# Optimization experiments

Measured on AMD Instinct MI355X. Metric: run time of the kernel, lower is better.

## Reference

```python
import jax, jax.numpy as jnp
import numpy as np

B, S, D = 1, 2048, 4096
H, KV = 32, 8
HD = D // H  # 128
NEG = -1e9


def _rope(t, cos, sin):
    # t: [B,S,h,HD]; cos/sin: [S,HD//2] -> broadcast [1,S,1,HD//2]
    tr = t[..., 0::2]
    ti = t[..., 1::2]
    c = cos[None, :, None, :]
    s = sin[None, :, None, :]
    out_r = tr * c - ti * s
    out_i = tr * s + ti * c
    # interleave back: (..., HD//2, 2) -> (..., HD)
    return jnp.stack([out_r, out_i], axis=-1).reshape(t.shape)


def setup_inputs() -> dict:
    key = jax.random.key(0)
    ks = jax.random.split(key, 5)
    w_scale = 0.02
    x = jax.random.normal(ks[0], (B, S, D), dtype=jnp.float32)
    wq = jax.random.normal(ks[1], (H * HD, D), dtype=jnp.float32) * w_scale
    wk = jax.random.normal(ks[2], (KV * HD, D), dtype=jnp.float32) * w_scale
    wv = jax.random.normal(ks[3], (KV * HD, D), dtype=jnp.float32) * w_scale
    wo = jax.random.normal(ks[4], (D, H * HD), dtype=jnp.float32) * w_scale
    # RoPE tables (theta = 10000)
    inv_freq = 1.0 / (10000.0 ** (np.arange(0, HD, 2, dtype=np.float32) / HD))
    angles = np.arange(S, dtype=np.float32)[:, None] * inv_freq[None, :]  # [S, HD//2]
    freqs_cos = jnp.asarray(np.cos(angles))
    freqs_sin = jnp.asarray(np.sin(angles))
    # causal additive mask [1,1,S,S]
    causal = jnp.tril(jnp.ones((S, S), dtype=bool))
    mask = jnp.where(causal, 0.0, NEG).astype(jnp.float32)[None, None]
    return {"x": x, "wq": wq, "wk": wk, "wv": wv, "wo": wo,
            "freqs_cos": freqs_cos, "freqs_sin": freqs_sin, "mask": mask}


def reference(x, wq, wk, wv, wo, freqs_cos, freqs_sin, mask):
    b, s, d = x.shape
    q = (x @ wq.T).reshape(b, s, H, HD)
    k = (x @ wk.T).reshape(b, s, KV, HD)
    v = (x @ wv.T).reshape(b, s, KV, HD)
    q = _rope(q, freqs_cos, freqs_sin)
    k = _rope(k, freqs_cos, freqs_sin)
    rep = H // KV
    k = jnp.repeat(k, rep, axis=2)  # [b,s,H,HD]
    v = jnp.repeat(v, rep, axis=2)
    scores = jnp.einsum('bshd,bthd->bhst', q, k) / jnp.sqrt(jnp.float32(HD))
    scores = scores + mask
    attn = jax.nn.softmax(scores, axis=-1)
    out = jnp.einsum('bhst,bthd->bshd', attn, v).reshape(b, s, H * HD)
    return out @ wo.T
```

## Files before the change

### kernel.cpp

```cpp
#include <hip/hip_runtime.h>
#include <hip/hip_bf16.h>
#include <math.h>

#define SEQ 2048
#define DIM 4096
#define NH 32
#define NKV 8
#define HD 128
#define KVD 1024
#define SCALE 0.08838834764831845f
#define NEGBIG -1000000000.0f

typedef __bf16 bf16;
typedef __attribute__((ext_vector_type(4))) __bf16 bf16x4;
typedef __attribute__((ext_vector_type(8))) __bf16 bf16x8;
typedef __attribute__((ext_vector_type(4))) float f32x4;

__device__ __forceinline__ void async_g2l16(const bf16* g, bf16* l) {
  __builtin_amdgcn_global_load_lds(
      (const __attribute__((address_space(1))) void*)g,
      (__attribute__((address_space(3))) void*)l,
      16, 0, 0);
}

#define SEG_X  2097152
#define SEG_WQ 4194304
#define SEG_WK 1048576
#define C0 SEG_X
#define C1 (C0 + SEG_WQ)
#define C2 (C1 + SEG_WK)
#define C3 (C2 + SEG_WK)
#define C4 (C3 + SEG_WQ)

__global__ void cast_all_kernel(const float* __restrict__ x,
                                const float* __restrict__ wq,
                                const float* __restrict__ wk,
                                const float* __restrict__ wv,
                                const float* __restrict__ wo,
                                bf16* __restrict__ xb, bf16* __restrict__ wqb,
                                bf16* __restrict__ wkb, bf16* __restrict__ wvb,
                                bf16* __restrict__ wob) {
  int i = blockIdx.x * 256 + threadIdx.x;
  const float* src; bf16* dst; int j;
  if (i < C0)      { src = x;  dst = xb;  j = i; }
  else if (i < C1) { src = wq; dst = wqb; j = i - C0; }
  else if (i < C2) { src = wk; dst = wkb; j = i - C1; }
  else if (i < C3) { src = wv; dst = wvb; j = i - C2; }
  else             { src = wo; dst = wob; j = i - C3; }
  float4 v = ((const float4*)src)[j];
  bf16x4 o;
  o[0] = (bf16)v.x; o[1] = (bf16)v.y; o[2] = (bf16)v.z; o[3] = (bf16)v.w;
  ((bf16x4*)dst)[j] = o;
}

#define BAR()       asm volatile("s_barrier" ::: "memory")
#define FENCE4()    asm volatile("s_waitcnt vmcnt(4)" ::: "memory")
#define FENCE_ALL() asm volatile("s_waitcnt vmcnt(0)" ::: "memory")

#define MFMAQ(AH, BC, MO, NO)                                              \
  _Pragma("unroll") for (int m2 = 0; m2 < 4; ++m2)                         \
  _Pragma("unroll") for (int n2 = 0; n2 < 2; ++n2)                         \
  _Pragma("unroll") for (int kk = 0; kk < 2; ++kk)                         \
    acc[(MO) + m2][(NO) + n2] = __builtin_amdgcn_mfma_f32_16x16x32_bf16(   \
        (AH)[m2][kk], (BC)[n2][kk], acc[(MO) + m2][(NO) + n2], 0, 0, 0);

__device__ __forceinline__ void gemm256_core(
    const bf16* __restrict__ Ag,
    const bf16* __restrict__ Bg,
    f32x4 acc[8][4])
{
  __shared__ __align__(16) bf16 As[2 * 256 * 64];
  __shared__ __align__(16) bf16 Bs[2 * 256 * 64];

  const int tid  = threadIdx.x;
  const int lane = tid & 63;
  const int w    = tid >> 6;
  const int l15  = lane & 15;
  const int quad = lane >> 4;
  const int wr2  = (w >> 2) * 128;
  const int wc2  = (w & 3) * 64;

  const int srow = w * 8 + (lane >> 3);
  const int sg8  = ((lane & 7) ^ (lane >> 3)) * 8;
  const bf16* gA = Ag + (size_t)srow * DIM + sg8;
  const bf16* gB = Bg + (size_t)srow * DIM + sg8;
  bf16* lA = As + w * 512;
  bf16* lB = Bs + w * 512;

  const int g0   = (quad ^ (l15 & 7)) * 8;
  const int g1   = g0 ^ 32;
  const int aOff = (wr2 + l15) * 64;
  const int bOff = (wc2 + l15) * 64;

#define STAGE_A(b, kt)                                                     \
  { _Pragma("unroll") for (int hh = 0; hh < 2; ++hh)                       \
    _Pragma("unroll") for (int j = 0; j < 2; ++j)                          \
      async_g2l16(gA + (size_t)(hh * 128 + j * 64) * DIM + (kt) * 64,      \
                  lA + (b) * 16384 + (hh * 128 + j * 64) * 64); }
#define STAGE_B0(b, kt)                                                    \
  { _Pragma("unroll") for (int j = 0; j < 2; ++j)                          \
      async_g2l16(gB + (size_t)(j * 64) * DIM + (kt) * 64,                 \
                  lB + (b) * 16384 + (j * 64) * 64); }
#define STAGE_B1(b, kt)                                                    \
  { _Pragma("unroll") for (int j = 0; j < 2; ++j)                          \
      async_g2l16(gB + (size_t)(128 + j * 64) * DIM + (kt) * 64,           \
                  lB + (b) * 16384 + (128 + j * 64) * 64); }

#define LDA(b, rh, m2, gk) \
  (*(const bf16x8*)(As + (b) * 16384 + aOff + (rh) * 4096 + (m2) * 1024 + (gk)))
#define LDB(b, ch, n2, gk) \
  (*(const bf16x8*)(Bs + (b) * 16384 + bOff + (ch) * 2048 + (n2) * 1024 + (gk)))

  const f32x4 vz = {0.f, 0.f, 0.f, 0.f};
#pragma unroll
  for (int mi = 0; mi < 8; ++mi)
#pragma unroll
    for (int ni = 0; ni < 4; ++ni) acc[mi][ni] = vz;

  STAGE_A(0, 0); STAGE_B0(0, 0); STAGE_B1(0, 0);
  STAGE_B0(1, 1); STAGE_B1(1, 1);
  FENCE4();
  BAR();

  for (int i = 0; i < 32; ++i) {
    const int ktn0 = (2 * i + 2 > 63) ? 63 : 2 * i + 2;
    const int ktn1 = (2 * i + 3 > 63) ? 63 : 2 * i + 3;
    {
      bf16x8 aH[4][2], bC0[2][2], bC1[2][2];
#pragma unroll
      for (int m2 = 0; m2 < 4; ++m2) { aH[m2][0] = LDA(0, 0, m2, g0); aH[m2][1] = LDA(0, 0, m2, g1); }
#pragma unroll
      for (int n2 = 0; n2 < 2; ++n2) { bC0[n2][0] = LDB(0, 0, n2, g0); bC0[n2][1] = LDB(0, 0, n2, g1); }
      STAGE_A(1, 2 * i + 1);
      BAR(); __builtin_amdgcn_s_setprio(1);
      MFMAQ(aH, bC0, 0, 0);
      __builtin_amdgcn_s_setprio(0); BAR();
#pragma unroll
      for (int n2 = 0; n2 < 2; ++n2) { bC1[n2][0] = LDB(0, 1, n2, g0); bC1[n2][1] = LDB(0, 1, n2, g1); }
      BAR(); __builtin_amdgcn_s_setprio(1);
      MFMAQ(aH, bC1, 0, 2);
      __builtin_amdgcn_s_setprio(0); BAR();
#pragma unroll
      for (int m2 = 0; m2 < 4; ++m2) { aH[m2][0] = LDA(0, 1, m2, g0); aH[m2][1] = LDA(0, 1, m2, g1); }
      STAGE_B0(0, ktn0);
      BAR(); __builtin_amdgcn_s_setprio(1);
      MFMAQ(aH, bC1, 4, 2);
      __builtin_amdgcn_s_setprio(0); BAR();
      STAGE_B1(0, ktn0);
      FENCE4();
      BAR(); __builtin_amdgcn_s_setprio(1);
      MFMAQ(aH, bC0, 4, 0);
      __builtin_amdgcn_s_setprio(0); BAR();
    }
    {
      bf16x8 aH[4][2], bC0[2][2], bC1[2][2];
#pragma unroll
      for (int m2 = 0; m2 < 4; ++m2) { aH[m2][0] = LDA(1, 0, m2, g0); aH[m2][1] = LDA(1, 0, m2, g1); }
#pragma unroll
      for (int n2 = 0; n2 < 2; ++n2) { bC0[n2][0] = LDB(1, 0, n2, g0); bC0[n2][1] = LDB(1, 0, n2, g1); }
      STAGE_A(0, ktn0);
      BAR(); __builtin_amdgcn_s_setprio(1);
      MFMAQ(aH, bC0, 0, 0);
      __builtin_amdgcn_s_setprio(0); BAR();
#pragma unroll
      for (int n2 = 0; n2 < 2; ++n2) { bC1[n2][0] = LDB(1, 1, n2, g0); bC1[n2][1] = LDB(1, 1, n2, g1); }
      BAR(); __builtin_amdgcn_s_setprio(1);
      MFMAQ(aH, bC1, 0, 2);
      __builtin_amdgcn_s_setprio(0); BAR();
#pragma unroll
      for (int m2 = 0; m2 < 4; ++m2) { aH[m2][0] = LDA(1, 1, m2, g0); aH[m2][1] = LDA(1, 1, m2, g1); }
      STAGE_B0(1, ktn1);
      BAR(); __builtin_amdgcn_s_setprio(1);
      MFMAQ(aH, bC1, 4, 2);
      __builtin_amdgcn_s_setprio(0); BAR();
      STAGE_B1(1, ktn1);
      FENCE4();
      BAR(); __builtin_amdgcn_s_setprio(1);
      MFMAQ(aH, bC0, 4, 0);
      __builtin_amdgcn_s_setprio(0); BAR();
    }
  }
  FENCE_ALL();
}

__global__ __launch_bounds__(512, 2) void qkv256_kernel(
    const bf16* __restrict__ xb, const bf16* __restrict__ wqb,
    const bf16* __restrict__ wkb, const bf16* __restrict__ wvb,
    const float* __restrict__ fc, const float* __restrict__ fs,
    bf16* __restrict__ Qb, bf16* __restrict__ Kb, bf16* __restrict__ Vt)
{
  const int bid   = blockIdx.x;
  const int mTile = bid & 7;
  const int nTile = bid >> 3;
  const bf16* Bg;
  if (nTile < 16)      Bg = wqb + (size_t)nTile * 256 * DIM;
  else if (nTile < 20) Bg = wkb + (size_t)(nTile - 16) * 256 * DIM;
  else                 Bg = wvb + (size_t)(nTile - 20) * 256 * DIM;

  f32x4 acc[8][4];
  gemm256_core(xb + (size_t)mTile * 256 * DIM, Bg, acc);

  const int tid  = threadIdx.x;
  const int lane = tid & 63;
  const int w    = tid >> 6;
  const int l15  = lane & 15;
  const int quad = lane >> 4;
  const int wr2  = (w >> 2) * 128;
  const int wc2  = (w & 3) * 64;
  const int sBase = mTile * 256 + wr2 + quad * 4;
  const int nBase = nTile * 256 + wc2;

  if (nTile < 20) {
    const bool isQ = nTile < 16;
    bf16* dst      = isQ ? Qb : Kb;
    const int ldd  = isQ ? DIM : KVD;
    const float sc = isQ ? SCALE : 1.0f;
    const int cOff = isQ ? nBase : nBase - 4096;
    const int odd  = l15 & 1;
#pragma unroll
    for (int mi = 0; mi < 8; ++mi)
#pragma unroll
      for (int ni = 0; ni < 4; ++ni) {
        const int n    = nBase + ni * 16 + l15;
        const int fidx = (n >> 1) & 63;
        const int col  = cOff + ni * 16 + l15;
#pragma unroll
        for (int r = 0; r < 4; ++r) {
          const int s = sBase + mi * 16 + r;
          float v  = acc[mi][ni][r];
          float pv = __shfl_xor(v, 1, 64);
          float c  = fc[s * 64 + fidx];
          float sn = fs[s * 64 + fidx];
          float o  = odd ? (pv * sn + v * c) : (v * c - pv * sn);
          dst[(size_t)s * ldd + col] = (bf16)(o * sc);
        }
      }
  } else {
    const int vBase = nBase - 5120;
#pragma unroll
    for (int mi = 0; mi < 8; ++mi) {
      const int sb = sBase + mi * 16;
#pragma unroll
      for (int ni = 0; ni < 4; ++ni) {
        const int nv = vBase + ni * 16 + l15;
        const int t = nv >> 7, d = nv & 127;
        bf16x4 pv;
#pragma unroll
        for (int r = 0; r < 4; ++r) pv[r] = (bf16)acc[mi][ni][r];
        *(bf16x4*)(Vt + ((size_t)t * HD + d) * SEQ + sb) = pv;
      }
    }
  }
}

__global__ __launch_bounds__(512, 2) void out256_kernel(
    const bf16* __restrict__ attnb, const bf16* __restrict__ wob,
    float* __restrict__ out)
{
  const int bid   = blockIdx.x;
  const int mTile = bid & 7;
  const int nTile = bid >> 3;

  f32x4 acc[8][4];
  gemm256_core(attnb + (size_t)mTile * 256 * DIM,
               wob + (size_t)nTile * 256 * DIM, acc);

  const int tid  = threadIdx.x;
  const int lane = tid & 63;
  const int w    = tid >> 6;
  const int l15  = lane & 15;
  const int quad = lane >> 4;
  const int wr2  = (w >> 2) * 128;
  const int wc2  = (w & 3) * 64;
  const int sBase = mTile * 256 + wr2 + quad * 4;
#pragma unroll
  for (int mi = 0; mi < 8; ++mi)
#pragma unroll
    for (int ni = 0; ni < 4; ++ni) {
      const int col = nTile * 256 + wc2 + ni * 16 + l15;
#pragma unroll
      for (int r = 0; r < 4; ++r)
        out[(size_t)(sBase + mi * 16 + r) * DIM + col] = acc[mi][ni][r];
    }
}

__global__ __launch_bounds__(256, 2) void attn_kernel(
    const bf16* __restrict__ Qb, const bf16* __restrict__ Kb,
    const bf16* __restrict__ Vt, bf16* __restrict__ attnb)
{
  __shared__ __align__(16) bf16 Ks[64 * 128];
  __shared__ __align__(16) bf16 Vs[128 * 64];
  __shared__ __align__(16) bf16 Ps[128 * 64];

  const int b    = blockIdx.x;
  const int half = b >> 8;
  const int r8   = b & 255;
  const int h    = (half << 4) | (r8 >> 4);
  const int qt   = half ? (r8 & 15) : 15 - (r8 & 15);
  const int kvh  = h >> 2;
  const int qbase = qt * 128;

  const int tid  = threadIdx.x;
  const int lane = tid & 63;
  const int w    = tid >> 6;
  const int l15  = lane & 15;
  const int quad = lane >> 4;

  bf16x8 qfrag[2][4];
#pragma unroll
  for (int n = 0; n < 2; ++n) {
    int q = qbase + w * 32 + n * 16 + l15;
#pragma unroll
    for (int ks = 0; ks < 4; ++ks)
      qfrag[n][ks] = *(const bf16x8*)(Qb + (size_t)q * DIM + h * HD +
                                      ks * 32 + quad * 8);
  }

  const f32x4 vzero = {0.f, 0.f, 0.f, 0.f};
  f32x4 oacc[8][2];
#pragma unroll
  for (int dm = 0; dm < 8; ++dm)
#pragma unroll
    for (int n = 0; n < 2; ++n) oacc[dm][n] = vzero;
  float m_run[2] = {-1e30f, -1e30f};
  float l_run[2] = {0.f, 0.f};

  const int nkt = 2 * (qt + 1);
  for (int kt = 0; kt < nkt; ++kt) {
    const int kbase = kt * 64;

    __syncthreads();
#pragma unroll
    for (int t = 0; t < 4; ++t) {
      int kr0 = w * 16 + t * 4;
      int krow = kr0 + (lane >> 4);
      int kg = (lane & 15) ^ (krow & 7);
      async_g2l16(Kb + (size_t)(kbase + krow) * KVD + kvh * HD + kg * 8,
                  Ks + kr0 * 128);
      int vr0 = w * 32 + t * 8;
      int d = vr0 + (lane >> 3);
      int vg = (lane & 7) ^ (d & 7);
      async_g2l16(Vt + ((size_t)kvh * HD + d) * SEQ + kbase + vg * 8,
                  Vs + vr0 * 64);
    }
    __syncthreads();

    f32x4 sacc[4][2];
#pragma unroll
    for (int kg = 0; kg < 4; ++kg)
#pragma unroll
      for (int n = 0; n < 2; ++n) sacc[kg][n] = vzero;
#pragma unroll
    for (int kg = 0; kg < 4; ++kg) {
      bf16x8 kf[4];
#pragma unroll
      for (int ks = 0; ks < 4; ++ks) {
        int row = kg * 16 + l15;
        kf[ks] = *(const bf16x8*)(Ks + row * 128 +
                                  (((ks * 4 + quad) ^ (row & 7)) * 8));
      }
#pragma unroll
      for (int n = 0; n < 2; ++n)
#pragma unroll
        for (int ks = 0; ks < 4; ++ks)
          sacc[kg][n] = __builtin_amdgcn_mfma_f32_16x16x32_bf16(
              kf[ks], qfrag[n][ks], sacc[kg][n], 0, 0, 0);
    }

#pragma unroll
    for (int n = 0; n < 2; ++n) {
      const int qloc = w * 32 + n * 16 + l15;
      const int qglob = qbase + qloc;
      if (kbase + 63 > qbase + w * 32 + n * 16) {
#pragma unroll
        for (int kg = 0; kg < 4; ++kg)
#pragma unroll
          for (int r = 0; r < 4; ++r) {
            int key = kbase + kg * 16 + quad * 4 + r;
            if (key > qglob) sacc[kg][n][r] = NEGBIG;
          }
      }
      float mx = -1e30f;
#pragma unroll
      for (int kg = 0; kg < 4; ++kg)
#pragma unroll
        for (int r = 0; r < 4; ++r) mx = fmaxf(mx, sacc[kg][n][r]);
      mx = fmaxf(mx, __shfl_xor(mx, 16, 64));
      mx = fmaxf(mx, __shfl_xor(mx, 32, 64));
      float mnew = fmaxf(m_run[n], mx);
      float alpha = __expf(m_run[n] - mnew);
      m_run[n] = mnew;
      float rs = 0.f;
#pragma unroll
      for (int kg = 0; kg < 4; ++kg) {
        bf16x4 pk;
#pragma unroll
        for (int r = 0; r < 4; ++r) {
          float p = __expf(sacc[kg][n][r] - mnew);
          rs += p;
          pk[r] = (bf16)p;
        }
        int g16 = (kg * 2 + (quad >> 1)) ^ (qloc & 7);
        *(bf16x4*)(Ps + qloc * 64 + g16 * 8 + (quad & 1) * 4) = pk;
      }
      rs += __shfl_xor(rs, 16, 64);
      rs += __shfl_xor(rs, 32, 64);
      l_run[n] = alpha * l_run[n] + rs;
#pragma unroll
      for (int dm = 0; dm < 8; ++dm)
#pragma unroll
        for (int r = 0; r < 4; ++r) oacc[dm][n][r] *= alpha;
    }

    bf16x8 pf[2][2];
#pragma unroll
    for (int kk = 0; kk < 2; ++kk)
#pragma unroll
      for (int n = 0; n < 2; ++n) {
        int qloc = w * 32 + n * 16 + l15;
        pf[kk][n] = *(const bf16x8*)(Ps + qloc * 64 +
                                     (((kk * 4 + quad) ^ (qloc & 7)) * 8));
      }
#pragma unroll
    for (int dm = 0; dm < 8; ++dm) {
#pragma unroll
      for (int kk = 0; kk < 2; ++kk) {
        int d = dm * 16 + l15;
        bf16x8 vf = *(const bf16x8*)(Vs + d * 64 +
                                     (((kk * 4 + quad) ^ (d & 7)) * 8));
#pragma unroll
        for (int n = 0; n < 2; ++n)
          oacc[dm][n] = __builtin_amdgcn_mfma_f32_16x16x32_bf16(
              vf, pf[kk][n], oacc[dm][n], 0, 0, 0);
      }
    }
  }

#pragma unroll
  for (int n = 0; n < 2; ++n) {
    float inv = 1.0f / l_run[n];
    int q = qbase + w * 32 + n * 16 + l15;
#pragma unroll
    for (int dm = 0; dm < 8; ++dm) {
      bf16x4 ov;
#pragma unroll
      for (int r = 0; r < 4; ++r) ov[r] = (bf16)(oacc[dm][n][r] * inv);
      *(bf16x4*)(attnb + (size_t)q * DIM + h * HD + dm * 16 + quad * 4) = ov;
    }
  }
}

extern "C" void kernel_launch(void* const* d_in, const int* in_sizes, int n_in,
                              void* d_out, int out_size, void* d_ws, size_t ws_size,
                              hipStream_t stream) {
  const float* x  = (const float*)d_in[0];
  const float* wq = (const float*)d_in[1];
  const float* wk = (const float*)d_in[2];
  const float* wv = (const float*)d_in[3];
  const float* wo = (const float*)d_in[4];
  const float* fc = (const float*)d_in[5];
  const float* fs = (const float*)d_in[6];
  float* out = (float*)d_out;

  size_t off = 0;
  char* wsb = (char*)d_ws;
  auto take = [&](size_t bytes) -> void* {
    void* p = wsb + off;
    off += (bytes + 255) & ~(size_t)255;
    return p;
  };
  bf16*  xb    = (bf16*)take((size_t)SEQ * DIM * 2);
  bf16*  wqb   = (bf16*)take((size_t)DIM * DIM * 2);
  bf16*  wkb   = (bf16*)take((size_t)KVD * DIM * 2);
  bf16*  wvb   = (bf16*)take((size_t)KVD * DIM * 2);
  bf16*  wob   = (bf16*)take((size_t)DIM * DIM * 2);
  bf16*  Qb    = (bf16*)take((size_t)SEQ * DIM * 2);
  bf16*  Kb    = (bf16*)take((size_t)SEQ * KVD * 2);
  bf16*  Vt    = (bf16*)take((size_t)NKV * HD * SEQ * 2);
  bf16*  attnb = (bf16*)take((size_t)SEQ * DIM * 2);

  cast_all_kernel<<<C4 / 256, 256, 0, stream>>>(x, wq, wk, wv, wo,
                                                xb, wqb, wkb, wvb, wob);

  qkv256_kernel<<<dim3(192), 512, 0, stream>>>(xb, wqb, wkb, wvb,
                                               fc, fs, Qb, Kb, Vt);

  attn_kernel<<<dim3(512), 256, 0, stream>>>(Qb, Kb, Vt, attnb);

  out256_kernel<<<dim3(128), 512, 0, stream>>>(attnb, wob, out);
}
```

Measured before the change: 511.7 us.

## Narrow GEMM N-tiles so QKV and output projections launch 256 blocks

```diff
diff --git a/kernel.cpp b/kernel.cpp
--- a/kernel.cpp
+++ b/kernel.cpp
@@ -26,11 +26,11 @@
 #define SEG_X  2097152
 #define SEG_WQ 4194304
 #define SEG_WK 1048576
-#define C0 SEG_X
-#define C1 (C0 + SEG_WQ)
-#define C2 (C1 + SEG_WK)
-#define C3 (C2 + SEG_WK)
-#define C4 (C3 + SEG_WQ)
+#define C0SEG SEG_X
+#define C1SEG (C0SEG + SEG_WQ)
+#define C2SEG (C1SEG + SEG_WK)
+#define C3SEG (C2SEG + SEG_WK)
+#define C4SEG (C3SEG + SEG_WQ)
 
 __global__ void cast_all_kernel(const float* __restrict__ x,
                                 const float* __restrict__ wq,
@@ -42,11 +42,11 @@
                                 bf16* __restrict__ wob) {
   int i = blockIdx.x * 256 + threadIdx.x;
   const float* src; bf16* dst; int j;
-  if (i < C0)      { src = x;  dst = xb;  j = i; }
-  else if (i < C1) { src = wq; dst = wqb; j = i - C0; }
-  else if (i < C2) { src = wk; dst = wkb; j = i - C1; }
-  else if (i < C3) { src = wv; dst = wvb; j = i - C2; }
-  else             { src = wo; dst = wob; j = i - C3; }
+  if (i < C0SEG)      { src = x;  dst = xb;  j = i; }
+  else if (i < C1SEG) { src = wq; dst = wqb; j = i - C0SEG; }
+  else if (i < C2SEG) { src = wk; dst = wkb; j = i - C1SEG; }
+  else if (i < C3SEG) { src = wv; dst = wvb; j = i - C2SEG; }
+  else                { src = wo; dst = wob; j = i - C3SEG; }
   float4 v = ((const float4*)src)[j];
   bf16x4 o;
   o[0] = (bf16)v.x; o[1] = (bf16)v.y; o[2] = (bf16)v.z; o[3] = (bf16)v.w;
@@ -54,23 +54,18 @@
 }
 
 #define BAR()       asm volatile("s_barrier" ::: "memory")
-#define FENCE4()    asm volatile("s_waitcnt vmcnt(4)" ::: "memory")
 #define FENCE_ALL() asm volatile("s_waitcnt vmcnt(0)" ::: "memory")
 
-#define MFMAQ(AH, BC, MO, NO)                                              \
-  _Pragma("unroll") for (int m2 = 0; m2 < 4; ++m2)                         \
-  _Pragma("unroll") for (int n2 = 0; n2 < 2; ++n2)                         \
-  _Pragma("unroll") for (int kk = 0; kk < 2; ++kk)                         \
-    acc[(MO) + m2][(NO) + n2] = __builtin_amdgcn_mfma_f32_16x16x32_bf16(   \
-        (AH)[m2][kk], (BC)[n2][kk], acc[(MO) + m2][(NO) + n2], 0, 0, 0);
-
+template<int NF>
 __device__ __forceinline__ void gemm256_core(
     const bf16* __restrict__ Ag,
     const bf16* __restrict__ Bg,
-    f32x4 acc[8][4])
+    f32x4 acc[8][NF])
 {
+  constexpr int C0F  = NF - (NF >> 1);
+  constexpr int BUFB = NF * 4096;
   __shared__ __align__(16) bf16 As[2 * 256 * 64];
-  __shared__ __align__(16) bf16 Bs[2 * 256 * 64];
+  __shared__ __align__(16) bf16 Bs[2 * BUFB];
 
   const int tid  = threadIdx.x;
   const int lane = tid & 63;
@@ -78,7 +73,7 @@
   const int l15  = lane & 15;
   const int quad = lane >> 4;
   const int wr2  = (w >> 2) * 128;
-  const int wc2  = (w & 3) * 64;
+  const int wc3  = (w & 3) * (16 * NF);
 
   const int srow = w * 8 + (lane >> 3);
   const int sg8  = ((lane & 7) ^ (lane >> 3)) * 8;
@@ -90,115 +85,119 @@
   const int g0   = (quad ^ (l15 & 7)) * 8;
   const int g1   = g0 ^ 32;
   const int aOff = (wr2 + l15) * 64;
-  const int bOff = (wc2 + l15) * 64;
-
-#define STAGE_A(b, kt)                                                     \
-  { _Pragma("unroll") for (int hh = 0; hh < 2; ++hh)                       \
-    _Pragma("unroll") for (int j = 0; j < 2; ++j)                          \
-      async_g2l16(gA + (size_t)(hh * 128 + j * 64) * DIM + (kt) * 64,      \
-                  lA + (b) * 16384 + (hh * 128 + j * 64) * 64); }
-#define STAGE_B0(b, kt)                                                    \
-  { _Pragma("unroll") for (int j = 0; j < 2; ++j)                          \
-      async_g2l16(gB + (size_t)(j * 64) * DIM + (kt) * 64,                 \
-                  lB + (b) * 16384 + (j * 64) * 64); }
-#define STAGE_B1(b, kt)                                                    \
-  { _Pragma("unroll") for (int j = 0; j < 2; ++j)                          \
-      async_g2l16(gB + (size_t)(128 + j * 64) * DIM + (kt) * 64,           \
-                  lB + (b) * 16384 + (128 + j * 64) * 64); }
-
-#define LDA(b, rh, m2, gk) \
-  (*(const bf16x8*)(As + (b) * 16384 + aOff + (rh) * 4096 + (m2) * 1024 + (gk)))
-#define LDB(b, ch, n2, gk) \
-  (*(const bf16x8*)(Bs + (b) * 16384 + bOff + (ch) * 2048 + (n2) * 1024 + (gk)))
+  const int bOff = (wc3 + l15) * 64;
+
+  auto stageA = [&](int b, int kt) {
+#pragma unroll
+    for (int j = 0; j < 4; ++j)
+      async_g2l16(gA + (size_t)(j * 64) * DIM + kt * 64,
+                  lA + b * 16384 + j * 4096);
+  };
+  auto stageB = [&](int b, int kt) {
+#pragma unroll
+    for (int j = 0; j < NF; ++j)
+      async_g2l16(gB + (size_t)(j * 64) * DIM + kt * 64,
+                  lB + b * BUFB + j * 4096);
+  };
+  auto fence_steady = [] {
+    if constexpr (NF == 3) asm volatile("s_waitcnt vmcnt(7)" ::: "memory");
+    else                   asm volatile("s_waitcnt vmcnt(6)" ::: "memory");
+  };
 
   const f32x4 vz = {0.f, 0.f, 0.f, 0.f};
 #pragma unroll
   for (int mi = 0; mi < 8; ++mi)
 #pragma unroll
-    for (int ni = 0; ni < 4; ++ni) acc[mi][ni] = vz;
-
-  STAGE_A(0, 0); STAGE_B0(0, 0); STAGE_B1(0, 0);
-  STAGE_B0(1, 1); STAGE_B1(1, 1);
-  FENCE4();
+    for (int ni = 0; ni < NF; ++ni) acc[mi][ni] = vz;
+
+  auto ktile = [&](int b, int kt2) {
+    const bf16* Ab = As + b * 16384;
+    const bf16* Bb = Bs + b * BUFB;
+    bf16x8 aH[4][2], bc0[C0F][2], bc1[2];
+#pragma unroll
+    for (int m2 = 0; m2 < 4; ++m2) {
+      aH[m2][0] = *(const bf16x8*)(Ab + aOff + m2 * 1024 + g0);
+      aH[m2][1] = *(const bf16x8*)(Ab + aOff + m2 * 1024 + g1);
+    }
+#pragma unroll
+    for (int n = 0; n < C0F; ++n) {
+      bc0[n][0] = *(const bf16x8*)(Bb + bOff + n * 1024 + g0);
+      bc0[n][1] = *(const bf16x8*)(Bb + bOff + n * 1024 + g1);
+    }
+    BAR(); __builtin_amdgcn_s_setprio(1);
+#pragma unroll
+    for (int m2 = 0; m2 < 4; ++m2)
+#pragma unroll
+      for (int n = 0; n < C0F; ++n)
+#pragma unroll
+        for (int kk = 0; kk < 2; ++kk)
+          acc[m2][n] = __builtin_amdgcn_mfma_f32_16x16x32_bf16(
+              aH[m2][kk], bc0[n][kk], acc[m2][n], 0, 0, 0);
+    __builtin_amdgcn_s_setprio(0); BAR();
+    bc1[0] = *(const bf16x8*)(Bb + bOff + C0F * 1024 + g0);
+    bc1[1] = *(const bf16x8*)(Bb + bOff + C0F * 1024 + g1);
+    BAR(); __builtin_amdgcn_s_setprio(1);
+#pragma unroll
+    for (int m2 = 0; m2 < 4; ++m2)
+#pragma unroll
+      for (int kk = 0; kk < 2; ++kk)
+        acc[m2][C0F] = __builtin_amdgcn_mfma_f32_16x16x32_bf16(
+            aH[m2][kk], bc1[kk], acc[m2][C0F], 0, 0, 0);
+    __builtin_amdgcn_s_setprio(0); BAR();
+#pragma unroll
+    for (int m2 = 0; m2 < 4; ++m2) {
+      aH[m2][0] = *(const bf16x8*)(Ab + aOff + 4096 + m2 * 1024 + g0);
+      aH[m2][1] = *(const bf16x8*)(Ab + aOff + 4096 + m2 * 1024 + g1);
+    }
+    stageB(b, kt2);
+    BAR(); __builtin_amdgcn_s_setprio(1);
+#pragma unroll
+    for (int m2 = 0; m2 < 4; ++m2)
+#pragma unroll
+      for (int kk = 0; kk < 2; ++kk)
+        acc[4 + m2][C0F] = __builtin_amdgcn_mfma_f32_16x16x32_bf16(
+            aH[m2][kk], bc1[kk], acc[4 + m2][C0F], 0, 0, 0);
+    __builtin_amdgcn_s_setprio(0); BAR();
+    stageA(b, kt2);
+    fence_steady();
+    BAR(); __builtin_amdgcn_s_setprio(1);
+#pragma unroll
+    for (int m2 = 0; m2 < 4; ++m2)
+#pragma unroll
+      for (int n = 0; n < C0F; ++n)
+#pragma unroll
+        for (int kk = 0; kk < 2; ++kk)
+          acc[4 + m2][n] = __builtin_amdgcn_mfma_f32_16x16x32_bf16(
+              aH[m2][kk], bc0[n][kk], acc[4 + m2][n], 0, 0, 0);
+    __builtin_amdgcn_s_setprio(0); BAR();
+  };
+
+  stageB(0, 0); stageA(0, 0); stageB(1, 1); stageA(1, 1);
+  fence_steady();
   BAR();
 
-  for (int i = 0; i < 32; ++i) {
-    const int ktn0 = (2 * i + 2 > 63) ? 63 : 2 * i + 2;
-    const int ktn1 = (2 * i + 3 > 63) ? 63 : 2 * i + 3;
-    {
-      bf16x8 aH[4][2], bC0[2][2], bC1[2][2];
-#pragma unroll
-      for (int m2 = 0; m2 < 4; ++m2) { aH[m2][0] = LDA(0, 0, m2, g0); aH[m2][1] = LDA(0, 0, m2, g1); }
-#pragma unroll
-      for (int n2 = 0; n2 < 2; ++n2) { bC0[n2][0] = LDB(0, 0, n2, g0); bC0[n2][1] = LDB(0, 0, n2, g1); }
-      STAGE_A(1, 2 * i + 1);
-      BAR(); __builtin_amdgcn_s_setprio(1);
-      MFMAQ(aH, bC0, 0, 0);
-      __builtin_amdgcn_s_setprio(0); BAR();
-#pragma unroll
-      for (int n2 = 0; n2 < 2; ++n2) { bC1[n2][0] = LDB(0, 1, n2, g0); bC1[n2][1] = LDB(0, 1, n2, g1); }
-      BAR(); __builtin_amdgcn_s_setprio(1);
-      MFMAQ(aH, bC1, 0, 2);
-      __builtin_amdgcn_s_setprio(0); BAR();
-#pragma unroll
-      for (int m2 = 0; m2 < 4; ++m2) { aH[m2][0] = LDA(0, 1, m2, g0); aH[m2][1] = LDA(0, 1, m2, g1); }
-      STAGE_B0(0, ktn0);
-      BAR(); __builtin_amdgcn_s_setprio(1);
-      MFMAQ(aH, bC1, 4, 2);
-      __builtin_amdgcn_s_setprio(0); BAR();
-      STAGE_B1(0, ktn0);
-      FENCE4();
-      BAR(); __builtin_amdgcn_s_setprio(1);
-      MFMAQ(aH, bC0, 4, 0);
-      __builtin_amdgcn_s_setprio(0); BAR();
-    }
-    {
-      bf16x8 aH[4][2], bC0[2][2], bC1[2][2];
-#pragma unroll
-      for (int m2 = 0; m2 < 4; ++m2) { aH[m2][0] = LDA(1, 0, m2, g0); aH[m2][1] = LDA(1, 0, m2, g1); }
-#pragma unroll
-      for (int n2 = 0; n2 < 2; ++n2) { bC0[n2][0] = LDB(1, 0, n2, g0); bC0[n2][1] = LDB(1, 0, n2, g1); }
-      STAGE_A(0, ktn0);
-      BAR(); __builtin_amdgcn_s_setprio(1);
-      MFMAQ(aH, bC0, 0, 0);
-      __builtin_amdgcn_s_setprio(0); BAR();
-#pragma unroll
-      for (int n2 = 0; n2 < 2; ++n2) { bC1[n2][0] = LDB(1, 1, n2, g0); bC1[n2][1] = LDB(1, 1, n2, g1); }
-      BAR(); __builtin_amdgcn_s_setprio(1);
-      MFMAQ(aH, bC1, 0, 2);
-      __builtin_amdgcn_s_setprio(0); BAR();
-#pragma unroll
-      for (int m2 = 0; m2 < 4; ++m2) { aH[m2][0] = LDA(1, 1, m2, g0); aH[m2][1] = LDA(1, 1, m2, g1); }
-      STAGE_B0(1, ktn1);
-      BAR(); __builtin_amdgcn_s_setprio(1);
-      MFMAQ(aH, bC1, 4, 2);
-      __builtin_amdgcn_s_setprio(0); BAR();
-      STAGE_B1(1, ktn1);
-      FENCE4();
-      BAR(); __builtin_amdgcn_s_setprio(1);
-      MFMAQ(aH, bC0, 4, 0);
-      __builtin_amdgcn_s_setprio(0); BAR();
-    }
+#pragma unroll 1
+  for (int t = 0; t < 64; t += 2) {
+    const int k2a = (t + 2 < 64) ? t + 2 : 63;
+    const int k2b = (t + 3 < 64) ? t + 3 : 63;
+    ktile(0, k2a);
+    ktile(1, k2b);
   }
   FENCE_ALL();
 }
 
 __global__ __launch_bounds__(512, 2) void qkv256_kernel(
-    const bf16* __restrict__ xb, const bf16* __restrict__ wqb,
-    const bf16* __restrict__ wkb, const bf16* __restrict__ wvb,
+    const bf16* __restrict__ xb, const bf16* __restrict__ wqkv,
     const float* __restrict__ fc, const float* __restrict__ fs,
     bf16* __restrict__ Qb, bf16* __restrict__ Kb, bf16* __restrict__ Vt)
 {
   const int bid   = blockIdx.x;
   const int mTile = bid & 7;
   const int nTile = bid >> 3;
-  const bf16* Bg;
-  if (nTile < 16)      Bg = wqb + (size_t)nTile * 256 * DIM;
-  else if (nTile < 20) Bg = wkb + (size_t)(nTile - 16) * 256 * DIM;
-  else                 Bg = wvb + (size_t)(nTile - 20) * 256 * DIM;
-
-  f32x4 acc[8][4];
-  gemm256_core(xb + (size_t)mTile * 256 * DIM, Bg, acc);
+
+  f32x4 acc[8][3];
+  gemm256_core<3>(xb + (size_t)mTile * 256 * DIM,
+                  wqkv + (size_t)nTile * 192 * DIM, acc);
 
   const int tid  = threadIdx.x;
   const int lane = tid & 63;
@@ -206,24 +205,24 @@
   const int l15  = lane & 15;
   const int quad = lane >> 4;
   const int wr2  = (w >> 2) * 128;
-  const int wc2  = (w & 3) * 64;
+  const int wc3  = (w & 3) * 48;
   const int sBase = mTile * 256 + wr2 + quad * 4;
-  const int nBase = nTile * 256 + wc2;
-
-  if (nTile < 20) {
-    const bool isQ = nTile < 16;
-    bf16* dst      = isQ ? Qb : Kb;
-    const int ldd  = isQ ? DIM : KVD;
-    const float sc = isQ ? SCALE : 1.0f;
-    const int cOff = isQ ? nBase : nBase - 4096;
-    const int odd  = l15 & 1;
-#pragma unroll
-    for (int mi = 0; mi < 8; ++mi)
-#pragma unroll
-      for (int ni = 0; ni < 4; ++ni) {
-        const int n    = nBase + ni * 16 + l15;
-        const int fidx = (n >> 1) & 63;
-        const int col  = cOff + ni * 16 + l15;
+  const int nBase = nTile * 192 + wc3;
+  const int odd  = l15 & 1;
+
+#pragma unroll
+  for (int ni = 0; ni < 3; ++ni) {
+    const int c16 = nBase + ni * 16;
+    const int col = c16 + l15;
+    if (c16 < 5120) {
+      const bool isQ = c16 < 4096;
+      bf16* dst      = isQ ? Qb : Kb;
+      const int ldd  = isQ ? DIM : KVD;
+      const float sc = isQ ? SCALE : 1.0f;
+      const int cc   = isQ ? col : col - 4096;
+      const int fidx = (col >> 1) & 63;
+#pragma unroll
+      for (int mi = 0; mi < 8; ++mi) {
 #pragma unroll
         for (int r = 0; r < 4; ++r) {
           const int s = sBase + mi * 16 + r;
@@ -232,22 +231,18 @@
           float c  = fc[s * 64 + fidx];
           float sn = fs[s * 64 + fidx];
           float o  = odd ? (pv * sn + v * c) : (v * c - pv * sn);
-          dst[(size_t)s * ldd + col] = (bf16)(o * sc);
+          dst[(size_t)s * ldd + cc] = (bf16)(o * sc);
         }
       }
-  } else {
-    const int vBase = nBase - 5120;
-#pragma unroll
-    for (int mi = 0; mi < 8; ++mi) {
-      const int sb = sBase + mi * 16;
-#pragma unroll
-      for (int ni = 0; ni < 4; ++ni) {
-        const int nv = vBase + ni * 16 + l15;
-        const int t = nv >> 7, d = nv & 127;
+    } else {
+      const int cv = col - 5120;
+      const int t = cv >> 7, d = cv & 127;
+#pragma unroll
+      for (int mi = 0; mi < 8; ++mi) {
         bf16x4 pv;
 #pragma unroll
         for (int r = 0; r < 4; ++r) pv[r] = (bf16)acc[mi][ni][r];
-        *(bf16x4*)(Vt + ((size_t)t * HD + d) * SEQ + sb) = pv;
+        *(bf16x4*)(Vt + ((size_t)t * HD + d) * SEQ + sBase + mi * 16) = pv;
       }
     }
   }
@@ -261,9 +256,9 @@
   const int mTile = bid & 7;
   const int nTile = bid >> 3;
 
-  f32x4 acc[8][4];
-  gemm256_core(attnb + (size_t)mTile * 256 * DIM,
-               wob + (size_t)nTile * 256 * DIM, acc);
+  f32x4 acc[8][2];
+  gemm256_core<2>(attnb + (size_t)mTile * 256 * DIM,
+                  wob + (size_t)nTile * 128 * DIM, acc);
 
   const int tid  = threadIdx.x;
   const int lane = tid & 63;
@@ -271,13 +266,14 @@
   const int l15  = lane & 15;
   const int quad = lane >> 4;
   const int wr2  = (w >> 2) * 128;
-  const int wc2  = (w & 3) * 64;
+  const int wc3  = (w & 3) * 32;
   const int sBase = mTile * 256 + wr2 + quad * 4;
+  const int cBase = nTile * 128 + wc3;
 #pragma unroll
   for (int mi = 0; mi < 8; ++mi)
 #pragma unroll
-    for (int ni = 0; ni < 4; ++ni) {
-      const int col = nTile * 256 + wc2 + ni * 16 + l15;
+    for (int ni = 0; ni < 2; ++ni) {
+      const int col = cBase + ni * 16 + l15;
 #pragma unroll
       for (int r = 0; r < 4; ++r)
         out[(size_t)(sBase + mi * 16 + r) * DIM + col] = acc[mi][ni][r];
@@ -479,13 +475,12 @@
   bf16*  Vt    = (bf16*)take((size_t)NKV * HD * SEQ * 2);
   bf16*  attnb = (bf16*)take((size_t)SEQ * DIM * 2);
 
-  cast_all_kernel<<<C4 / 256, 256, 0, stream>>>(x, wq, wk, wv, wo,
-                                                xb, wqb, wkb, wvb, wob);
-
-  qkv256_kernel<<<dim3(192), 512, 0, stream>>>(xb, wqb, wkb, wvb,
-                                               fc, fs, Qb, Kb, Vt);
+  cast_all_kernel<<<C4SEG / 256, 256, 0, stream>>>(x, wq, wk, wv, wo,
+                                                   xb, wqb, wkb, wvb, wob);
+
+  qkv256_kernel<<<dim3(256), 512, 0, stream>>>(xb, wqb, fc, fs, Qb, Kb, Vt);
 
   attn_kernel<<<dim3(512), 256, 0, stream>>>(Qb, Kb, Vt, attnb);
 
-  out256_kernel<<<dim3(128), 512, 0, stream>>>(attnb, wob, out);
-}
+  out256_kernel<<<dim3(256), 512, 0, stream>>>(attnb, wob, out);
+}
```

Result: faster. 491.6 us (-3.9%).

## Overlap wo cast with QKV GEMM and retile output GEMM to 128x128

Applied to the files above, without the earlier changes.

```diff
diff --git a/kernel.cpp b/kernel.cpp
--- a/kernel.cpp
+++ b/kernel.cpp
@@ -26,27 +26,23 @@
 #define SEG_X  2097152
 #define SEG_WQ 4194304
 #define SEG_WK 1048576
-#define C0 SEG_X
-#define C1 (C0 + SEG_WQ)
-#define C2 (C1 + SEG_WK)
-#define C3 (C2 + SEG_WK)
-#define C4 (C3 + SEG_WQ)
+#define CX0 SEG_X
+#define CX1 (CX0 + SEG_WQ)
+#define CX2 (CX1 + SEG_WK)
+#define CX3 (CX2 + SEG_WK)
 
 __global__ void cast_all_kernel(const float* __restrict__ x,
                                 const float* __restrict__ wq,
                                 const float* __restrict__ wk,
                                 const float* __restrict__ wv,
-                                const float* __restrict__ wo,
                                 bf16* __restrict__ xb, bf16* __restrict__ wqb,
-                                bf16* __restrict__ wkb, bf16* __restrict__ wvb,
-                                bf16* __restrict__ wob) {
+                                bf16* __restrict__ wkb, bf16* __restrict__ wvb) {
   int i = blockIdx.x * 256 + threadIdx.x;
   const float* src; bf16* dst; int j;
-  if (i < C0)      { src = x;  dst = xb;  j = i; }
-  else if (i < C1) { src = wq; dst = wqb; j = i - C0; }
-  else if (i < C2) { src = wk; dst = wkb; j = i - C1; }
-  else if (i < C3) { src = wv; dst = wvb; j = i - C2; }
-  else             { src = wo; dst = wob; j = i - C3; }
+  if (i < CX0)      { src = x;  dst = xb;  j = i; }
+  else if (i < CX1) { src = wq; dst = wqb; j = i - CX0; }
+  else if (i < CX2) { src = wk; dst = wkb; j = i - CX1; }
+  else              { src = wv; dst = wvb; j = i - CX2; }
   float4 v = ((const float4*)src)[j];
   bf16x4 o;
   o[0] = (bf16)v.x; o[1] = (bf16)v.y; o[2] = (bf16)v.z; o[3] = (bf16)v.w;
@@ -186,10 +182,21 @@
 __global__ __launch_bounds__(512, 2) void qkv256_kernel(
     const bf16* __restrict__ xb, const bf16* __restrict__ wqb,
     const bf16* __restrict__ wkb, const bf16* __restrict__ wvb,
+    const float* __restrict__ wo, bf16* __restrict__ wob,
     const float* __restrict__ fc, const float* __restrict__ fs,
     bf16* __restrict__ Qb, bf16* __restrict__ Kb, bf16* __restrict__ Vt)
 {
-  const int bid   = blockIdx.x;
+  const int bid = blockIdx.x;
+  const int tid = threadIdx.x;
+  if (bid >= 192) {
+    for (int j = (bid - 192) * 512 + tid; j < SEG_WQ; j += 64 * 512) {
+      float4 v = ((const float4*)wo)[j];
+      bf16x4 o;
+      o[0] = (bf16)v.x; o[1] = (bf16)v.y; o[2] = (bf16)v.z; o[3] = (bf16)v.w;
+      ((bf16x4*)wob)[j] = o;
+    }
+    return;
+  }
   const int mTile = bid & 7;
   const int nTile = bid >> 3;
   const bf16* Bg;
@@ -200,7 +207,6 @@
   f32x4 acc[8][4];
   gemm256_core(xb + (size_t)mTile * 256 * DIM, Bg, acc);
 
-  const int tid  = threadIdx.x;
   const int lane = tid & 63;
   const int w    = tid >> 6;
   const int l15  = lane & 15;
@@ -253,35 +259,94 @@
   }
 }
 
-__global__ __launch_bounds__(512, 2) void out256_kernel(
-    const bf16* __restrict__ attnb, const bf16* __restrict__ wob,
-    float* __restrict__ out)
+__device__ __forceinline__ void gemm128_core(
+    const bf16* __restrict__ A, int lda,
+    const bf16* __restrict__ B, int ldb,
+    int K, int mBase, f32x4 acc[4][4])
 {
-  const int bid   = blockIdx.x;
-  const int mTile = bid & 7;
-  const int nTile = bid >> 3;
-
-  f32x4 acc[8][4];
-  gemm256_core(attnb + (size_t)mTile * 256 * DIM,
-               wob + (size_t)nTile * 256 * DIM, acc);
+  __shared__ __align__(16) bf16 As[128 * 32];
+  __shared__ __align__(16) bf16 Bs[128 * 32];
 
   const int tid  = threadIdx.x;
   const int lane = tid & 63;
   const int w    = tid >> 6;
   const int l15  = lane & 15;
   const int quad = lane >> 4;
-  const int wr2  = (w >> 2) * 128;
-  const int wc2  = (w & 3) * 64;
-  const int sBase = mTile * 256 + wr2 + quad * 4;
-#pragma unroll
-  for (int mi = 0; mi < 8; ++mi)
+  const int wr   = (w >> 1) * 64;
+  const int wc   = (w & 1) * 64;
+
+  const int srow = lane >> 2;
+  const int kswz = ((lane & 3) ^ ((srow >> 1) & 3)) * 8;
+  const bf16* gA0 = A + (size_t)(mBase + w * 16 + srow) * lda + kswz;
+  const bf16* gA1 = gA0 + (size_t)64 * lda;
+  const bf16* gB0 = B + (size_t)(w * 16 + srow) * ldb + kswz;
+  const bf16* gB1 = gB0 + (size_t)64 * ldb;
+  bf16* lA0 = As + w * 512;
+  bf16* lA1 = As + (w + 4) * 512;
+  bf16* lB0 = Bs + w * 512;
+  bf16* lB1 = Bs + (w + 4) * 512;
+
+  const f32x4 vzero = {0.f, 0.f, 0.f, 0.f};
+#pragma unroll
+  for (int mi = 0; mi < 4; ++mi)
+#pragma unroll
+    for (int ni = 0; ni < 4; ++ni) acc[mi][ni] = vzero;
+
+  const int rsw = ((l15 >> 1) & 3);
+
+  for (int k0 = 0; k0 < K; k0 += 32) {
+    __syncthreads();
+    async_g2l16(gA0 + k0, lA0);
+    async_g2l16(gA1 + k0, lA1);
+    async_g2l16(gB0 + k0, lB0);
+    async_g2l16(gB1 + k0, lB1);
+    __syncthreads();
+
+    bf16x8 a[4], b[4];
+#pragma unroll
+    for (int mi = 0; mi < 4; ++mi)
+      a[mi] = *(const bf16x8*)(As + (wr + mi * 16 + l15) * 32 +
+                               ((quad ^ rsw) * 8));
+#pragma unroll
+    for (int ni = 0; ni < 4; ++ni)
+      b[ni] = *(const bf16x8*)(Bs + (wc + ni * 16 + l15) * 32 +
+                               ((quad ^ rsw) * 8));
+#pragma unroll
+    for (int mi = 0; mi < 4; ++mi)
+#pragma unroll
+      for (int ni = 0; ni < 4; ++ni)
+        acc[mi][ni] = __builtin_amdgcn_mfma_f32_16x16x32_bf16(
+            a[mi], b[ni], acc[mi][ni], 0, 0, 0);
+  }
+}
+
+__global__ __launch_bounds__(256, 2) void out_gemm_kernel(
+    const bf16* __restrict__ attnb, const bf16* __restrict__ wob,
+    float* __restrict__ out)
+{
+  const int mBase = blockIdx.y * 128;
+  f32x4 acc[4][4];
+  gemm128_core(attnb, DIM, wob + (size_t)blockIdx.x * 128 * DIM, DIM, DIM,
+               mBase, acc);
+
+  const int tid  = threadIdx.x;
+  const int lane = tid & 63;
+  const int w    = tid >> 6;
+  const int l15  = lane & 15;
+  const int quad = lane >> 4;
+  const int wr   = (w >> 1) * 64;
+  const int wc   = (w & 1) * 64;
+#pragma unroll
+  for (int mi = 0; mi < 4; ++mi) {
+    int row = mBase + wr + mi * 16 + quad * 4;
 #pragma unroll
     for (int ni = 0; ni < 4; ++ni) {
-      const int col = nTile * 256 + wc2 + ni * 16 + l15;
+      int col = blockIdx.x * 128 + wc + ni * 16 + l15;
 #pragma unroll
       for (int r = 0; r < 4; ++r)
-        out[(size_t)(sBase + mi * 16 + r) * DIM + col] = acc[mi][ni][r];
-    }
+        out[(size_t)(row + r) * DIM + col] = acc[mi][ni][r];
+    }
+  }
 }
 
 __global__ __launch_bounds__(256, 2) void attn_kernel(
@@ -479,13 +544,13 @@
   bf16*  Vt    = (bf16*)take((size_t)NKV * HD * SEQ * 2);
   bf16*  attnb = (bf16*)take((size_t)SEQ * DIM * 2);
 
-  cast_all_kernel<<<C4 / 256, 256, 0, stream>>>(x, wq, wk, wv, wo,
-                                                xb, wqb, wkb, wvb, wob);
-
-  qkv256_kernel<<<dim3(192), 512, 0, stream>>>(xb, wqb, wkb, wvb,
+  cast_all_kernel<<<CX3 / 256, 256, 0, stream>>>(x, wq, wk, wv,
+                                                 xb, wqb, wkb, wvb);
+
+  qkv256_kernel<<<dim3(256), 512, 0, stream>>>(xb, wqb, wkb, wvb, wo, wob,
                                                fc, fs, Qb, Kb, Vt);
 
   attn_kernel<<<dim3(512), 256, 0, stream>>>(Qb, Kb, Vt, attnb);
 
-  out256_kernel<<<dim3(128), 512, 0, stream>>>(attnb, wob, out);
-}
+  out_gemm_kernel<<<dim3(32, 16), 256, 0, stream>>>(attnb, wob, out);
+}
```

New measurement: 462.1 us. 1.11x faster.
